# Performance work log

Hardware: AMD Instinct MI355X
Metric: run time of the kernel (lower is better)

## Reference

```python
import jax, jax.numpy as jnp
import numpy as np

D_MODEL = 1024
N_HEAD = 16
HEAD_DIM = D_MODEL // N_HEAD


def setup_inputs() -> dict:
    key = jax.random.key(0)
    k1, k2, k3 = jax.random.split(key, 3)
    x = jax.random.normal(k1, (2, 2048, D_MODEL), dtype=jnp.float32)
    w_qkv = jax.random.normal(k2, (D_MODEL, 3 * D_MODEL), dtype=jnp.float32) * (1.0 / np.sqrt(D_MODEL))
    w_proj = jax.random.normal(k3, (D_MODEL, D_MODEL), dtype=jnp.float32) * (1.0 / np.sqrt(D_MODEL))
    return {"x": x, "w_qkv": w_qkv, "w_proj": w_proj}


def reference(x, w_qkv, w_proj):
    bs, sl, dm = x.shape
    qkv = x @ w_qkv                                   # [B,S,3*D]
    qkv = qkv.reshape(bs, sl, 3, N_HEAD, HEAD_DIM)
    q, k, v = qkv[:, :, 0], qkv[:, :, 1], qkv[:, :, 2]  # [B,S,H,d]
    q = q.transpose(0, 2, 1, 3)                        # [B,H,S,d]
    k = k.transpose(0, 2, 1, 3)
    v = v.transpose(0, 2, 1, 3)
    sc = 1.0 / np.sqrt(HEAD_DIM).astype(np.float32)
    attn = jnp.einsum('bhqd,bhkd->bhqk', q, k) * sc    # [B,H,S,S]
    causal = jnp.tril(jnp.ones((sl, sl), dtype=bool))  # True = keep
    attn = jnp.where(causal, attn, -jnp.inf)
    w = jax.nn.softmax(attn, axis=-1)                  # [B,H,S,S] (dropout p=0)
    o = jnp.einsum('bhqk,bhkd->bhqd', w, v)            # [B,H,S,d]
    out = o.transpose(0, 2, 1, 3).reshape(bs, sl, dm)
    out = out @ w_proj
    return (out, w)
```

## Files before the change

### kernel.cpp

```cpp
#include <hip/hip_runtime.h>

typedef _Float16 half8 __attribute__((ext_vector_type(8)));
typedef float f32x4 __attribute__((ext_vector_type(4)));

__device__ __forceinline__ void gl2lds16(const _Float16* g, _Float16* l) {
  __builtin_amdgcn_global_load_lds((const __attribute__((address_space(1))) void*)g,
                                   (__attribute__((address_space(3))) void*)l, 16, 0, 0);
}

__global__ __launch_bounds__(256) void cvt_kernel(const float* __restrict__ in,
                                                  _Float16* __restrict__ out, int n) {
  int i = (blockIdx.x * 256 + threadIdx.x) * 8;
  if (i >= n) return;
  float4 a = *(const float4*)(in + i);
  float4 b = *(const float4*)(in + i + 4);
  half8 o;
  o[0] = (_Float16)a.x; o[1] = (_Float16)a.y; o[2] = (_Float16)a.z; o[3] = (_Float16)a.w;
  o[4] = (_Float16)b.x; o[5] = (_Float16)b.y; o[6] = (_Float16)b.z; o[7] = (_Float16)b.w;
  *(half8*)(out + i) = o;
}

__global__ __launch_bounds__(256) void cvtT_kernel(const float* __restrict__ in,
                                                   _Float16* __restrict__ out,
                                                   int K, int N) {
  __shared__ float Ts[64][65];
  const int k0 = blockIdx.y * 64, n0 = blockIdx.x * 64;
  const int t = threadIdx.x;
  const int r = t >> 4, c = (t & 15) * 4;
#pragma unroll
  for (int i = 0; i < 4; i++) {
    float4 v = *(const float4*)(in + (size_t)(k0 + r + i * 16) * N + n0 + c);
    Ts[r + i * 16][c] = v.x; Ts[r + i * 16][c + 1] = v.y;
    Ts[r + i * 16][c + 2] = v.z; Ts[r + i * 16][c + 3] = v.w;
  }
  __syncthreads();
  const int nl = t >> 2, kq = (t & 3) * 16;
  half8 o0, o1;
#pragma unroll
  for (int j = 0; j < 8; j++) {
    o0[j] = (_Float16)Ts[kq + j][nl];
    o1[j] = (_Float16)Ts[kq + 8 + j][nl];
  }
  *(half8*)(out + (size_t)(n0 + nl) * K + k0 + kq) = o0;
  *(half8*)(out + (size_t)(n0 + nl) * K + k0 + kq + 8) = o1;
}

__global__ __launch_bounds__(256) void vtrans_kernel(const _Float16* __restrict__ v,
                                                     _Float16* __restrict__ vt) {
  __shared__ _Float16 Ht[64][72];
  const int s0 = blockIdx.x * 64;
  const _Float16* vb = v + (size_t)blockIdx.y * 131072;
  _Float16* vtb = vt + (size_t)blockIdx.y * 131072;
  const int t = threadIdx.x;
  const int sl = t >> 3, dq = (t & 7) * 8;
  *(half8*)&Ht[sl][dq] = *(const half8*)(vb + (s0 + sl) * 64 + dq);
  *(half8*)&Ht[sl + 32][dq] = *(const half8*)(vb + (s0 + sl + 32) * 64 + dq);
  __syncthreads();
  const int dl = t >> 2, sq = (t & 3) * 16;
  half8 o0, o1;
#pragma unroll
  for (int j = 0; j < 8; j++) {
    o0[j] = Ht[sq + j][dl];
    o1[j] = Ht[sq + 8 + j][dl];
  }
  *(half8*)(vtb + (size_t)dl * 2048 + s0 + sq) = o0;
  *(half8*)(vtb + (size_t)dl * 2048 + s0 + sq + 8) = o1;
}

template <int MODE, int BN>
__global__ __launch_bounds__(256) void gemm16(const _Float16* __restrict__ A,
                                              const _Float16* __restrict__ B,
                                              float* __restrict__ Cf,
                                              _Float16* __restrict__ Ch,
                                              int M, int N, int K) {
  constexpr int MI = (BN == 128) ? 4 : 2;
  __shared__ __align__(16) _Float16 As[128 * 32];
  __shared__ __align__(16) _Float16 Bs[BN * 32];
  const int tid = threadIdx.x;
  const int lane = tid & 63;
  const int wid = tid >> 6;
  const int quad = lane >> 4;
  const int l16 = lane & 15;
  const int mbase = (BN == 128) ? (wid >> 1) * 64 : wid * 32;
  const int nbase = (BN == 128) ? (wid & 1) * 64 : 0;
  const int m0 = blockIdx.y * 128;
  const int n0 = blockIdx.x * BN;

  f32x4 acc[MI][4];
  const f32x4 fz = {0.f, 0.f, 0.f, 0.f};
#pragma unroll
  for (int i = 0; i < MI; i++)
#pragma unroll
    for (int j = 0; j < 4; j++) acc[i][j] = fz;

  const int srow = tid >> 2;
  const int kq = (tid & 3) * 8;

  for (int kt = 0; kt < K; kt += 32) {
    gl2lds16(A + (size_t)(m0 + srow) * K + kt + kq, &As[tid * 8]);
    gl2lds16(A + (size_t)(m0 + 64 + srow) * K + kt + kq, &As[2048 + tid * 8]);
    gl2lds16(B + (size_t)(n0 + srow) * K + kt + kq, &Bs[tid * 8]);
    if (BN == 128)
      gl2lds16(B + (size_t)(n0 + 64 + srow) * K + kt + kq, &Bs[2048 + tid * 8]);
    __syncthreads();
    half8 af[MI], bf[4];
#pragma unroll
    for (int mi = 0; mi < MI; mi++)
      af[mi] = *(const half8*)&As[(mbase + mi * 16 + l16) * 32 + quad * 8];
#pragma unroll
    for (int ni = 0; ni < 4; ni++)
      bf[ni] = *(const half8*)&Bs[(nbase + ni * 16 + l16) * 32 + quad * 8];
#pragma unroll
    for (int mi = 0; mi < MI; mi++)
#pragma unroll
      for (int ni = 0; ni < 4; ni++)
        acc[mi][ni] = __builtin_amdgcn_mfma_f32_16x16x32_f16(af[mi], bf[ni], acc[mi][ni], 0, 0, 0);
    __syncthreads();
  }

#pragma unroll
  for (int mi = 0; mi < MI; mi++)
#pragma unroll
    for (int ni = 0; ni < 4; ni++)
#pragma unroll
      for (int r = 0; r < 4; r++) {
        int row = m0 + mbase + mi * 16 + quad * 4 + r;
        int col = n0 + nbase + ni * 16 + l16;
        float v = acc[mi][ni][r];
        if (MODE == 0) {
          Cf[(size_t)row * N + col] = v;
        } else {
          int which = col >> 10, h = (col >> 6) & 15, d = col & 63;
          int b = row >> 11, s = row & 2047;
          Ch[((((size_t)(which * 2 + b) * 16 + h) * 2048) + s) * 64 + d] = (_Float16)v;
        }
      }
}

__global__ __launch_bounds__(256) void attn_kernel(const _Float16* __restrict__ qkv,
                                                   const _Float16* __restrict__ vt,
                                                   float* __restrict__ w_out,
                                                   _Float16* __restrict__ o_buf) {
  const int qt = blockIdx.x, bh = blockIdx.y;
  const int tid = threadIdx.x;
  const int lane = tid & 63;
  const int wid = tid >> 6;
  const int quad = lane >> 4;
  const int l16 = lane & 15;

  const _Float16* qp = qkv + (size_t)bh * 131072;
  const _Float16* kp = qp + 4194304;
  const _Float16* vtb = vt + (size_t)bh * 131072;

  __shared__ __align__(16) _Float16 Ks[2 * 64 * 32];
  __shared__ __align__(16) _Float16 Vs[2 * 64 * 32];
  __shared__ __align__(16) _Float16 Ps[64][72];

  const int qrow = qt * 64 + wid * 16 + l16;
  const half8 qa0 = *(const half8*)(qp + qrow * 64 + quad * 8);
  const half8 qa1 = *(const half8*)(qp + qrow * 64 + 32 + quad * 8);

  const int srow = tid >> 2;
  const int blk8 = (tid & 3) * 8;
  const float sc = 0.125f;
  const f32x4 fz = {0.f, 0.f, 0.f, 0.f};
  const int lrow0 = wid * 16 + quad * 4;

  float lsum[4] = {0.f, 0.f, 0.f, 0.f};

  for (int kt = 0; kt <= qt; kt++) {
    gl2lds16(kp + (size_t)(kt * 64 + srow) * 64 + blk8, &Ks[tid * 8]);
    gl2lds16(kp + (size_t)(kt * 64 + srow) * 64 + 32 + blk8, &Ks[2048 + tid * 8]);
    __syncthreads();
    f32x4 sacc[4];
#pragma unroll
    for (int ni = 0; ni < 4; ni++) {
      half8 kb0 = *(const half8*)&Ks[(ni * 16 + l16) * 32 + quad * 8];
      half8 kb1 = *(const half8*)&Ks[2048 + (ni * 16 + l16) * 32 + quad * 8];
      f32x4 s = fz;
      s = __builtin_amdgcn_mfma_f32_16x16x32_f16(qa0, kb0, s, 0, 0, 0);
      s = __builtin_amdgcn_mfma_f32_16x16x32_f16(qa1, kb1, s, 0, 0, 0);
      sacc[ni] = s;
    }
    if (kt < qt) {
#pragma unroll
      for (int ni = 0; ni < 4; ni++)
#pragma unroll
        for (int r = 0; r < 4; r++) lsum[r] += __expf(sacc[ni][r] * sc);
    } else {
#pragma unroll
      for (int ni = 0; ni < 4; ni++)
#pragma unroll
        for (int r = 0; r < 4; r++) {
          if (ni * 16 + l16 <= lrow0 + r) lsum[r] += __expf(sacc[ni][r] * sc);
        }
    }
    __syncthreads();
  }
  float invl[4];
#pragma unroll
  for (int r = 0; r < 4; r++) {
    float s = lsum[r];
    s += __shfl_xor(s, 1); s += __shfl_xor(s, 2);
    s += __shfl_xor(s, 4); s += __shfl_xor(s, 8);
    invl[r] = 1.0f / s;
  }

  f32x4 oacc[4];
#pragma unroll
  for (int di = 0; di < 4; di++) oacc[di] = fz;

  float* wbase = w_out + (size_t)bh * 4194304 + (size_t)qt * 64 * 2048;

  for (int kt = 0; kt < 32; kt++) {
    if (kt <= qt) {
      gl2lds16(kp + (size_t)(kt * 64 + srow) * 64 + blk8, &Ks[tid * 8]);
      gl2lds16(kp + (size_t)(kt * 64 + srow) * 64 + 32 + blk8, &Ks[2048 + tid * 8]);
      gl2lds16(vtb + (size_t)srow * 2048 + kt * 64 + blk8, &Vs[tid * 8]);
      gl2lds16(vtb + (size_t)srow * 2048 + kt * 64 + 32 + blk8, &Vs[2048 + tid * 8]);
      __syncthreads();
      f32x4 sacc[4];
#pragma unroll
      for (int ni = 0; ni < 4; ni++) {
        half8 kb0 = *(const half8*)&Ks[(ni * 16 + l16) * 32 + quad * 8];
        half8 kb1 = *(const half8*)&Ks[2048 + (ni * 16 + l16) * 32 + quad * 8];
        f32x4 s = fz;
        s = __builtin_amdgcn_mfma_f32_16x16x32_f16(qa0, kb0, s, 0, 0, 0);
        s = __builtin_amdgcn_mfma_f32_16x16x32_f16(qa1, kb1, s, 0, 0, 0);
        sacc[ni] = s;
      }
#pragma unroll
      for (int ni = 0; ni < 4; ni++)
#pragma unroll
        for (int r = 0; r < 4; r++) {
          int lrw = lrow0 + r;
          int col = ni * 16 + l16;
          float p = __expf(sacc[ni][r] * sc) * invl[r];
          if (kt == qt && col > lrw) p = 0.0f;
          wbase[(size_t)lrw * 2048 + kt * 64 + col] = p;
          Ps[lrw][col] = (_Float16)p;
        }
      __syncthreads();
#pragma unroll
      for (int kk = 0; kk < 2; kk++) {
        half8 pa = *(const half8*)&Ps[wid * 16 + l16][kk * 32 + quad * 8];
#pragma unroll
        for (int di = 0; di < 4; di++) {
          half8 vb = *(const half8*)&Vs[kk * 2048 + (di * 16 + l16) * 32 + quad * 8];
          oacc[di] = __builtin_amdgcn_mfma_f32_16x16x32_f16(pa, vb, oacc[di], 0, 0, 0);
        }
      }
      __syncthreads();
    } else {
      const int rr = tid >> 4;
      const int cc = (tid & 15) * 4;
      float* wz = wbase + (size_t)kt * 64 + cc;
#pragma unroll
      for (int p = 0; p < 4; p++)
        *(f32x4*)(wz + (size_t)(p * 16 + rr) * 2048) = fz;
    }
  }

  const int b = bh >> 4, h = bh & 15;
#pragma unroll
  for (int di = 0; di < 4; di++)
#pragma unroll
    for (int r = 0; r < 4; r++) {
      int s = qt * 64 + lrow0 + r;
      int d = di * 16 + l16;
      o_buf[((size_t)(b * 2048 + s) * 16 + h) * 64 + d] = (_Float16)oacc[di][r];
    }
}

extern "C" void kernel_launch(void* const* d_in, const int* in_sizes, int n_in,
                              void* d_out, int out_size, void* d_ws, size_t ws_size,
                              hipStream_t stream) {
  const float* x = (const float*)d_in[0];
  const float* w_qkv = (const float*)d_in[1];
  const float* w_proj = (const float*)d_in[2];
  float* out = (float*)d_out;
  float* w_attn = out + (size_t)4194304;

  char* ws = (char*)d_ws;
  _Float16* x16 = (_Float16*)ws;
  _Float16* wqkvT = (_Float16*)(ws + (size_t)(8 << 20));
  _Float16* wprojT = (_Float16*)(ws + (size_t)(14 << 20));
  _Float16* qkvb = (_Float16*)(ws + (size_t)(16 << 20));
  _Float16* vT = (_Float16*)(ws + (size_t)(40 << 20));
  _Float16* ob = (_Float16*)(ws + (size_t)(48 << 20));

  cvt_kernel<<<2048, 256, 0, stream>>>(x, x16, 4194304);
  cvtT_kernel<<<dim3(48, 16), 256, 0, stream>>>(w_qkv, wqkvT, 1024, 3072);
  cvtT_kernel<<<dim3(16, 16), 256, 0, stream>>>(w_proj, wprojT, 1024, 1024);

  gemm16<1, 128><<<dim3(24, 32), 256, 0, stream>>>(x16, wqkvT, nullptr, qkvb, 4096, 3072, 1024);
  vtrans_kernel<<<dim3(32, 32), 256, 0, stream>>>(qkvb + (size_t)2 * 4194304, vT);
  attn_kernel<<<dim3(32, 32), 256, 0, stream>>>(qkvb, vT, w_attn, ob);
  gemm16<0, 64><<<dim3(16, 32), 256, 0, stream>>>(ob, wprojT, out, nullptr, 4096, 1024, 1024);
}
```

Before: 722.0 us.

## Reverse query-tile order, vectorize weight stores, batch K tiles in softmax-sum pass

Blocks now take query tiles in reverse order so the longest causal rows are scheduled first. The masked upper triangle of the attention-weight output is zero-filled once up front with vector stores. The normalizer pass loads two K tiles per barrier, using the V buffer as the second K slot. The probability tile is written to global memory by reading the fp16 copy back from shared memory and storing it as contiguous float4 vectors, replacing the strided scalar stores. This makes the stored weights fp16-rounded, which is a small precision loss in the returned w, and adds extra shared-memory reads per tile.

```diff
diff --git a/kernel.cpp b/kernel.cpp
--- a/kernel.cpp
+++ b/kernel.cpp
@@ -141,7 +141,8 @@
                                                    const _Float16* __restrict__ vt,
                                                    float* __restrict__ w_out,
                                                    _Float16* __restrict__ o_buf) {
-  const int qt = blockIdx.x, bh = blockIdx.y;
+  const int qt = 31 - blockIdx.x;
+  const int bh = blockIdx.y;
   const int tid = threadIdx.x;
   const int lane = tid & 63;
   const int wid = tid >> 6;
@@ -156,6 +157,16 @@
   __shared__ __align__(16) _Float16 Vs[2 * 64 * 32];
   __shared__ __align__(16) _Float16 Ps[64][72];
 
+  float* wbase = w_out + (size_t)bh * 4194304 + (size_t)qt * 64 * 2048;
+  const f32x4 fz = {0.f, 0.f, 0.f, 0.f};
+
+  {
+    const int zrow = tid >> 2;
+    float* zr = wbase + (size_t)zrow * 2048;
+    for (int c = (qt + 1) * 64 + (tid & 3) * 4; c < 2048; c += 16)
+      *(f32x4*)(zr + c) = fz;
+  }
+
   const int qrow = qt * 64 + wid * 16 + l16;
   const half8 qa0 = *(const half8*)(qp + qrow * 64 + quad * 8);
   const half8 qa1 = *(const half8*)(qp + qrow * 64 + 32 + quad * 8);
@@ -163,16 +174,61 @@
   const int srow = tid >> 2;
   const int blk8 = (tid & 3) * 8;
   const float sc = 0.125f;
-  const f32x4 fz = {0.f, 0.f, 0.f, 0.f};
   const int lrow0 = wid * 16 + quad * 4;
+  const int grow0 = qt * 64 + lrow0;
 
   float lsum[4] = {0.f, 0.f, 0.f, 0.f};
 
-  for (int kt = 0; kt <= qt; kt++) {
+  int kt = 0;
+  while (kt <= qt) {
+    const bool two = (kt + 1 <= qt);
     gl2lds16(kp + (size_t)(kt * 64 + srow) * 64 + blk8, &Ks[tid * 8]);
     gl2lds16(kp + (size_t)(kt * 64 + srow) * 64 + 32 + blk8, &Ks[2048 + tid * 8]);
-    __syncthreads();
-    f32x4 sacc[4];
+    if (two) {
+      gl2lds16(kp + (size_t)((kt + 1) * 64 + srow) * 64 + blk8, &Vs[tid * 8]);
+      gl2lds16(kp + (size_t)((kt + 1) * 64 + srow) * 64 + 32 + blk8, &Vs[2048 + tid * 8]);
+    }
+    __syncthreads();
+#pragma unroll
+    for (int half = 0; half < 2; half++) {
+      if (half == 1 && !two) break;
+      const _Float16* buf = (half == 0) ? Ks : Vs;
+      const int tk = kt + half;
+#pragma unroll
+      for (int ni = 0; ni < 4; ni++) {
+        half8 kb0 = *(const half8*)&buf[(ni * 16 + l16) * 32 + quad * 8];
+        half8 kb1 = *(const half8*)&buf[2048 + (ni * 16 + l16) * 32 + quad * 8];
+        f32x4 s = fz;
+        s = __builtin_amdgcn_mfma_f32_16x16x32_f16(qa0, kb0, s, 0, 0, 0);
+        s = __builtin_amdgcn_mfma_f32_16x16x32_f16(qa1, kb1, s, 0, 0, 0);
+        const int gcol = tk * 64 + ni * 16 + l16;
+#pragma unroll
+        for (int r = 0; r < 4; r++)
+          lsum[r] += (gcol <= grow0 + r) ? __expf(s[r] * sc) : 0.f;
+      }
+    }
+    __syncthreads();
+    kt += two ? 2 : 1;
+  }
+  float invl[4];
+#pragma unroll
+  for (int r = 0; r < 4; r++) {
+    float s = lsum[r];
+    s += __shfl_xor(s, 1); s += __shfl_xor(s, 2);
+    s += __shfl_xor(s, 4); s += __shfl_xor(s, 8);
+    invl[r] = 1.0f / s;
+  }
+
+  f32x4 oacc[4];
+#pragma unroll
+  for (int di = 0; di < 4; di++) oacc[di] = fz;
+
+  for (int kt2 = 0; kt2 <= qt; kt2++) {
+    gl2lds16(kp + (size_t)(kt2 * 64 + srow) * 64 + blk8, &Ks[tid * 8]);
+    gl2lds16(kp + (size_t)(kt2 * 64 + srow) * 64 + 32 + blk8, &Ks[2048 + tid * 8]);
+    gl2lds16(vtb + (size_t)srow * 2048 + kt2 * 64 + blk8, &Vs[tid * 8]);
+    gl2lds16(vtb + (size_t)srow * 2048 + kt2 * 64 + 32 + blk8, &Vs[2048 + tid * 8]);
+    __syncthreads();
 #pragma unroll
     for (int ni = 0; ni < 4; ni++) {
       half8 kb0 = *(const half8*)&Ks[(ni * 16 + l16) * 32 + quad * 8];
@@ -180,85 +236,39 @@
       f32x4 s = fz;
       s = __builtin_amdgcn_mfma_f32_16x16x32_f16(qa0, kb0, s, 0, 0, 0);
       s = __builtin_amdgcn_mfma_f32_16x16x32_f16(qa1, kb1, s, 0, 0, 0);
-      sacc[ni] = s;
-    }
-    if (kt < qt) {
-#pragma unroll
-      for (int ni = 0; ni < 4; ni++)
-#pragma unroll
-        for (int r = 0; r < 4; r++) lsum[r] += __expf(sacc[ni][r] * sc);
-    } else {
-#pragma unroll
-      for (int ni = 0; ni < 4; ni++)
-#pragma unroll
-        for (int r = 0; r < 4; r++) {
-          if (ni * 16 + l16 <= lrow0 + r) lsum[r] += __expf(sacc[ni][r] * sc);
-        }
-    }
-    __syncthreads();
-  }
-  float invl[4];
-#pragma unroll
-  for (int r = 0; r < 4; r++) {
-    float s = lsum[r];
-    s += __shfl_xor(s, 1); s += __shfl_xor(s, 2);
-    s += __shfl_xor(s, 4); s += __shfl_xor(s, 8);
-    invl[r] = 1.0f / s;
-  }
-
-  f32x4 oacc[4];
-#pragma unroll
-  for (int di = 0; di < 4; di++) oacc[di] = fz;
-
-  float* wbase = w_out + (size_t)bh * 4194304 + (size_t)qt * 64 * 2048;
-
-  for (int kt = 0; kt < 32; kt++) {
-    if (kt <= qt) {
-      gl2lds16(kp + (size_t)(kt * 64 + srow) * 64 + blk8, &Ks[tid * 8]);
-      gl2lds16(kp + (size_t)(kt * 64 + srow) * 64 + 32 + blk8, &Ks[2048 + tid * 8]);
-      gl2lds16(vtb + (size_t)srow * 2048 + kt * 64 + blk8, &Vs[tid * 8]);
-      gl2lds16(vtb + (size_t)srow * 2048 + kt * 64 + 32 + blk8, &Vs[2048 + tid * 8]);
-      __syncthreads();
-      f32x4 sacc[4];
-#pragma unroll
-      for (int ni = 0; ni < 4; ni++) {
-        half8 kb0 = *(const half8*)&Ks[(ni * 16 + l16) * 32 + quad * 8];
-        half8 kb1 = *(const half8*)&Ks[2048 + (ni * 16 + l16) * 32 + quad * 8];
-        f32x4 s = fz;
-        s = __builtin_amdgcn_mfma_f32_16x16x32_f16(qa0, kb0, s, 0, 0, 0);
-        s = __builtin_amdgcn_mfma_f32_16x16x32_f16(qa1, kb1, s, 0, 0, 0);
-        sacc[ni] = s;
+      const int gcol = kt2 * 64 + ni * 16 + l16;
+#pragma unroll
+      for (int r = 0; r < 4; r++) {
+        float p = (gcol <= grow0 + r) ? __expf(s[r] * sc) * invl[r] : 0.f;
+        Ps[lrow0 + r][ni * 16 + l16] = (_Float16)p;
       }
-#pragma unroll
-      for (int ni = 0; ni < 4; ni++)
-#pragma unroll
-        for (int r = 0; r < 4; r++) {
-          int lrw = lrow0 + r;
-          int col = ni * 16 + l16;
-          float p = __expf(sacc[ni][r] * sc) * invl[r];
-          if (kt == qt && col > lrw) p = 0.0f;
-          wbase[(size_t)lrw * 2048 + kt * 64 + col] = p;
-          Ps[lrw][col] = (_Float16)p;
-        }
-      __syncthreads();
-#pragma unroll
-      for (int kk = 0; kk < 2; kk++) {
-        half8 pa = *(const half8*)&Ps[wid * 16 + l16][kk * 32 + quad * 8];
-#pragma unroll
-        for (int di = 0; di < 4; di++) {
-          half8 vb = *(const half8*)&Vs[kk * 2048 + (di * 16 + l16) * 32 + quad * 8];
-          oacc[di] = __builtin_amdgcn_mfma_f32_16x16x32_f16(pa, vb, oacc[di], 0, 0, 0);
-        }
+    }
+    __syncthreads();
+#pragma unroll
+    for (int kk = 0; kk < 2; kk++) {
+      half8 pa = *(const half8*)&Ps[wid * 16 + l16][kk * 32 + quad * 8];
+#pragma unroll
+      for (int di = 0; di < 4; di++) {
+        half8 vb = *(const half8*)&Vs[kk * 2048 + (di * 16 + l16) * 32 + quad * 8];
+        oacc[di] = __builtin_amdgcn_mfma_f32_16x16x32_f16(pa, vb, oacc[di], 0, 0, 0);
       }
-      __syncthreads();
-    } else {
-      const int rr = tid >> 4;
-      const int cc = (tid & 15) * 4;
-      float* wz = wbase + (size_t)kt * 64 + cc;
-#pragma unroll
-      for (int p = 0; p < 4; p++)
-        *(f32x4*)(wz + (size_t)(p * 16 + rr) * 2048) = fz;
-    }
+    }
+    {
+      const int wrow = tid >> 2;
+      const int wcol = (tid & 3) * 16;
+      half8 h0 = *(const half8*)&Ps[wrow][wcol];
+      half8 h1 = *(const half8*)&Ps[wrow][wcol + 8];
+      float* dst = wbase + (size_t)wrow * 2048 + kt2 * 64 + wcol;
+      f32x4 f0 = {(float)h0[0], (float)h0[1], (float)h0[2], (float)h0[3]};
+      f32x4 f1 = {(float)h0[4], (float)h0[5], (float)h0[6], (float)h0[7]};
+      f32x4 f2 = {(float)h1[0], (float)h1[1], (float)h1[2], (float)h1[3]};
+      f32x4 f3 = {(float)h1[4], (float)h1[5], (float)h1[6], (float)h1[7]};
+      *(f32x4*)dst = f0;
+      *(f32x4*)(dst + 4) = f1;
+      *(f32x4*)(dst + 8) = f2;
+      *(f32x4*)(dst + 12) = f3;
+    }
+    __syncthreads();
   }
 
   const int b = bh >> 4, h = bh & 15;
```

Result: slower. 768.3 us (+6.4%).
